# Kernel tuning notes

Hardware: AMD Instinct MI355X
Metric: run time of the kernel (lower is better)

## Reference

```python
import jax, jax.numpy as jnp
import numpy as np

S, G, NMUL, LENF = 730, 4000, 2, 15
NEARZERO = 1e-5

# param bounds (change_param_range: lb + raw*(ub-lb)), raw in [0,1]
HBV_LB = np.array([1., 50., .05, .01, .001, .2, 0., 0., -2.5, .5, 0., 0.], np.float32)
HBV_UB = np.array([6., 1000., .9, .5, .2, 1., 10., 100., 2.5, 10., .1, .2], np.float32)
EXP_LB = np.array([0., 100., 10., 0., 0., -3.], np.float32)
EXP_UB = np.array([.1, 1500., 50., 5., 3., 0.], np.float32)


def _descale(raw, lb, ub):
    # raw: [G, n_par, NMUL]
    return lb[None, :, None] + raw * (ub - lb)[None, :, None]


def _hbv(P, T, PET, ph):
    # ph: [G,12,NMUL]; order: beta fc k0 k1 k2 lp perc uzl tt cfmax cfr cwh
    beta, fc, k0, k1, k2, lp, perc, uzl, tt, cfmax, cfr, cwh = [ph[:, i, :] for i in range(12)]

    def step(carry, inp):
        sp, mw, sm, suz, slz = carry
        p, t, pet = inp
        rain = jnp.where(t >= tt, p, 0.)
        sp = sp + jnp.where(t < tt, p, 0.)
        melt = jnp.minimum(jnp.maximum(cfmax * (t - tt), 0.), sp)
        mw = mw + melt; sp = sp - melt
        refr = jnp.minimum(jnp.maximum(cfr * cfmax * (tt - t), 0.), mw)
        sp = sp + refr; mw = mw - refr
        tosoil = jnp.maximum(mw - cwh * sp, 0.)
        mw = mw - tosoil
        sw = jnp.clip((sm / fc) ** beta, 0., 1.)
        rech = (rain + tosoil) * sw
        sm = sm + rain + tosoil - rech
        excess = jnp.maximum(sm - fc, 0.); sm = sm - excess
        et = jnp.minimum(pet * jnp.clip(sm / (lp * fc), 0., 1.), sm)
        sm = jnp.maximum(sm - et, NEARZERO)
        suz = suz + rech + excess
        pa = jnp.minimum(perc, suz); suz = suz - pa
        q0 = k0 * jnp.maximum(suz - uzl, 0.); suz = suz - q0
        q1 = k1 * suz; suz = suz - q1
        slz = slz + pa
        q2 = k2 * slz; slz = slz - q2
        return (sp, mw, sm, suz, slz), q0 + q1 + q2

    z = jnp.full_like(fc, NEARZERO)
    init = (z, z, 0.5 * fc, z, z)
    _, q = jax.lax.scan(step, init, (P, T, PET))
    return q  # [S,G,NMUL]


def _exphydro(P, T, PET, pe):
    # pe: [G,6,NMUL]; order: f smax qmax df tmax tmin
    f, smax, qmax, df, tmax, tmin = [pe[:, i, :] for i in range(6)]

    def step(carry, inp):
        s0, s1 = carry
        p, t, pet = inp
        ps = jnp.where(t <= tmin, p, 0.)
        pr = p - ps
        melt = jnp.where(t > tmax, jnp.minimum(s0, df * (t - tmax)), 0.)
        s0 = s0 + ps - melt
        s1 = s1 + pr + melt
        qspill = jnp.maximum(s1 - smax, 0.); s1 = s1 - qspill
        et = jnp.minimum(pet * jnp.clip(s1 / smax, 0., 1.), s1); s1 = s1 - et
        qb = jnp.minimum(qmax * jnp.exp(-f * jnp.maximum(smax - s1, 0.)), s1)
        s1 = s1 - qb
        return (s0, s1), qspill + qb

    z = jnp.full_like(smax, NEARZERO)
    init = (z, 0.5 * smax)
    _, q = jax.lax.scan(step, init, (P, T, PET))
    return q  # [S,G,NMUL]


def _uh_gamma(a, b):
    # a,b: [G]; gamma-pdf unit hydrograph, lenF=LENF
    aa = jax.nn.relu(a) + 0.1
    th = jax.nn.relu(b) + 0.5
    t = jnp.arange(LENF, dtype=jnp.float32) + 0.5  # [LENF]
    logw = (-jax.scipy.special.gammaln(aa)[None, :] - aa[None, :] * jnp.log(th)[None, :]
            + (aa - 1.)[None, :] * jnp.log(t)[:, None] - t[:, None] / th[None, :])
    w = jnp.exp(logw)
    return w / w.sum(0, keepdims=True)  # [LENF,G]


def _route(q, w):
    # causal depthwise conv: out[t,g] = sum_k w[k,g] * q[t-k,g]
    qp = jnp.pad(q, ((LENF - 1, 0), (0, 0)))
    out = jnp.zeros_like(q)
    for k in range(LENF):
        out = out + w[k][None, :] * qp[LENF - 1 - k: LENF - 1 - k + q.shape[0]]
    return out


def setup_inputs() -> dict:
    key = jax.random.key(0)
    k1, k2 = jax.random.split(key)
    u = jax.random.uniform(k1, (S, G, 3), dtype=jnp.float32)
    # physical forcing ranges: prcp [0,10] mm/d, tmean [-10,20] C, pet [0,5] mm/d
    x = jnp.stack([u[..., 0] * 10., u[..., 1] * 30. - 10., u[..., 2] * 5.], axis=-1)
    raw_phy_static = jax.random.uniform(k2, (G, 18 * NMUL + 2), dtype=jnp.float32)
    return {"x": x, "raw_phy_static": raw_phy_static}


def reference(x, raw_phy_static):
    # unpack: [G, 18*NMUL] static block + 2 routing params
    static = raw_phy_static[:, :18 * NMUL].reshape(G, 18, NMUL)
    ph = _descale(static[:, :12, :], jnp.asarray(HBV_LB), jnp.asarray(HBV_UB))
    pe = _descale(static[:, 12:, :], jnp.asarray(EXP_LB), jnp.asarray(EXP_UB))
    route = raw_phy_static[:, 18 * NMUL:]
    rout_a = route[:, 0] * 2.9   # bounds [0, 2.9]
    rout_b = route[:, 1] * 6.5   # bounds [0, 6.5]

    P = jnp.broadcast_to(x[:, :, 0, None], (S, G, NMUL))
    T = jnp.broadcast_to(x[:, :, 1, None], (S, G, NMUL))
    PET = jnp.broadcast_to(x[:, :, 2, None], (S, G, NMUL))

    q_hbv = _hbv(P, T, PET, ph)
    q_exp = _exphydro(P, T, PET, pe)
    qsim = 0.5 * (q_hbv.mean(-1) + q_exp.mean(-1))  # blend over models, mean over nmul -> [S,G]

    w = _uh_gamma(rout_a, rout_b)
    return _route(qsim, w)  # [S,G] routed streamflow
```

## Files before the change

### kernel.cpp

```cpp
#include <hip/hip_runtime.h>

#define SS 730
#define GG 4000
#define LENF 15
#define PD 10
#define GPAD 4032
#define TT 10
#define QN ((size_t)SS * GG)

template<bool STORE4>
__global__ __launch_bounds__(64, 1) void hydro_scan(const float* __restrict__ x,
                                                    const float* __restrict__ raw,
                                                    float* __restrict__ qsim) {
    int tid = blockIdx.x * 64 + threadIdx.x;
    int g = tid % GPAD;
    int inst = tid / GPAD;
    if (g >= GG) return;
    int m = inst & 1;
    const float* xg = x + (size_t)g * 3;
    const float* pr = raw + (size_t)g * 38 + m;

    float* qp = qsim + (STORE4 ? (size_t)inst * QN : 0) + g;

    float pb[PD], tb[PD], eb[PD];
#pragma unroll
    for (int j = 0; j < PD; ++j) {
        const float* xn = xg + (size_t)j * (3 * GG);
        pb[j] = xn[0]; tb[j] = xn[1]; eb[j] = xn[2];
    }

    if (inst < 2) {
        float beta  = 1.0f   + pr[0]  * 5.0f;
        float fc    = 50.0f  + pr[2]  * 950.0f;
        float k0    = 0.05f  + pr[4]  * 0.85f;
        float k1    = 0.01f  + pr[6]  * 0.49f;
        float k2    = 0.001f + pr[8]  * 0.199f;
        float lp    = 0.2f   + pr[10] * 0.8f;
        float perc  =          pr[12] * 10.0f;
        float uzl   =          pr[14] * 100.0f;
        float tt    = -2.5f  + pr[16] * 5.0f;
        float cfmax = 0.5f   + pr[18] * 9.5f;
        float cfr   =          pr[20] * 0.1f;
        float cwh   =          pr[22] * 0.2f;
        float invfc   = 1.0f / fc;
        float invlpfc = 1.0f / (lp * fc);
        float cfrcf   = cfr * cfmax;

        float sp = 1e-5f, mw = 1e-5f, sm = 0.5f * fc, suz = 1e-5f, slz = 1e-5f;

        auto body = [&](float p, float tc, float pet) -> float {
            float sw = exp2f(beta * __log2f(sm * invfc));
            float rain = (tc >= tt) ? p : 0.0f;
            float snow = p - rain;
            sp += snow;
            float melt = fminf(fmaxf(cfmax * (tc - tt), 0.0f), sp);
            mw += melt; sp -= melt;
            float refr = fminf(fmaxf(cfrcf * (tt - tc), 0.0f), mw);
            sp += refr; mw -= refr;
            float tosoil = fmaxf(mw - cwh * sp, 0.0f);
            mw -= tosoil;
            float rt = rain + tosoil;
            float rech = rt * sw;
            sm += rt - rech;
            float excess = fmaxf(sm - fc, 0.0f);
            sm -= excess;
            float et = fminf(pet * fminf(sm * invlpfc, 1.0f), sm);
            sm = fmaxf(sm - et, 1e-5f);
            suz += rech + excess;
            float pa = fminf(perc, suz);
            suz -= pa;
            float q0 = k0 * fmaxf(suz - uzl, 0.0f);
            suz -= q0;
            float q1 = k1 * suz;
            suz -= q1;
            slz += pa;
            float q2 = k2 * slz;
            slz -= q2;
            return q0 + q1 + q2;
        };

        const float* xpre = xg + (size_t)PD * (3 * GG);
        for (int c = 0; c < SS / PD - 1; ++c) {
#pragma unroll
            for (int j = 0; j < PD; ++j) {
                float p = pb[j], tc = tb[j], pet = eb[j];
                pb[j] = xpre[0]; tb[j] = xpre[1]; eb[j] = xpre[2];
                xpre += 3 * GG;
                float q = body(p, tc, pet);
                if (STORE4) *qp = q; else atomicAdd(qp, 0.25f * q);
                qp += GG;
            }
        }
#pragma unroll
        for (int j = 0; j < PD; ++j) {
            float q = body(pb[j], tb[j], eb[j]);
            if (STORE4) *qp = q; else atomicAdd(qp, 0.25f * q);
            qp += GG;
        }
    } else {
        const float* pe = pr + 24;
        float f    =           pe[0]  * 0.1f;
        float smax = 100.0f  + pe[2]  * 1400.0f;
        float qmax = 10.0f   + pe[4]  * 40.0f;
        float df   =           pe[6]  * 5.0f;
        float tmax =           pe[8]  * 3.0f;
        float tmin = -3.0f   + pe[10] * 3.0f;
        float invsmax = 1.0f / smax;
        float fl = f * 1.44269504f;

        float s0 = 1e-5f, s1 = 0.5f * smax;

        auto body = [&](float p, float tc, float pet) -> float {
            float ps  = (tc <= tmin) ? p : 0.0f;
            float prr = p - ps;
            float mlt = (tc > tmax) ? fminf(s0, df * (tc - tmax)) : 0.0f;
            s0 += ps - mlt;
            s1 += prr + mlt;
            float qspill = fmaxf(s1 - smax, 0.0f);
            s1 -= qspill;
            float et = fminf(pet * (s1 * invsmax), s1);
            s1 -= et;
            float qb = fminf(qmax * exp2f(-fl * (smax - s1)), s1);
            s1 -= qb;
            return qspill + qb;
        };

        const float* xpre = xg + (size_t)PD * (3 * GG);
        for (int c = 0; c < SS / PD - 1; ++c) {
#pragma unroll
            for (int j = 0; j < PD; ++j) {
                float p = pb[j], tc = tb[j], pet = eb[j];
                pb[j] = xpre[0]; tb[j] = xpre[1]; eb[j] = xpre[2];
                xpre += 3 * GG;
                float q = body(p, tc, pet);
                if (STORE4) *qp = q; else atomicAdd(qp, 0.25f * q);
                qp += GG;
            }
        }
#pragma unroll
        for (int j = 0; j < PD; ++j) {
            float q = body(pb[j], tb[j], eb[j]);
            if (STORE4) *qp = q; else atomicAdd(qp, 0.25f * q);
            qp += GG;
        }
    }
}

__global__ __launch_bounds__(256) void uh_weights(const float* __restrict__ raw,
                                                  float* __restrict__ wbuf) {
    int g = blockIdx.x * 256 + threadIdx.x;
    if (g >= GG) return;
    float a = raw[(size_t)g * 38 + 36] * 2.9f;
    float b = raw[(size_t)g * 38 + 37] * 6.5f;
    float aa = fmaxf(a, 0.0f) + 0.1f;
    float th = fmaxf(b, 0.0f) + 0.5f;
    float am1 = aa - 1.0f;
    float invth = 1.0f / th;

    const float logt[LENF] = {
        -0.69314718f, 0.40546511f, 0.91629073f, 1.25276297f, 1.50407740f,
         1.70474809f, 1.87180218f, 2.01490302f, 2.14006616f, 2.25129180f,
         2.35137526f, 2.44234704f, 2.52572864f, 2.60268969f, 2.67414865f };

    float w[LENF];
    float s = 0.0f;
#pragma unroll
    for (int k = 0; k < LENF; ++k) {
        float tk = (float)k + 0.5f;
        w[k] = expf(am1 * logt[k] - tk * invth);
        s += w[k];
    }
    float scale = 0.25f / s;
#pragma unroll
    for (int k = 0; k < LENF; ++k)
        wbuf[(size_t)k * GG + g] = w[k] * scale;
}

template<int NB, bool WPRE>
__global__ __launch_bounds__(256) void hydro_route(const float* __restrict__ qsim,
                                                   const float* __restrict__ raw,
                                                   const float* __restrict__ wbuf,
                                                   float* __restrict__ out) {
    int idx = blockIdx.x * 256 + threadIdx.x;
    if (idx >= GG * (SS / TT)) return;
    int g = idx % GG;
    int c = idx / GG;
    int t0 = c * TT;

    float w[LENF];
    float scale;
    if (WPRE) {
#pragma unroll
        for (int k = 0; k < LENF; ++k)
            w[k] = wbuf[(size_t)k * GG + g];
        scale = 1.0f;
    } else {
        float a = raw[(size_t)g * 38 + 36] * 2.9f;
        float b = raw[(size_t)g * 38 + 37] * 6.5f;
        float aa = fmaxf(a, 0.0f) + 0.1f;
        float th = fmaxf(b, 0.0f) + 0.5f;
        float am1 = aa - 1.0f;
        float invth = 1.0f / th;
        const float logt[LENF] = {
            -0.69314718f, 0.40546511f, 0.91629073f, 1.25276297f, 1.50407740f,
             1.70474809f, 1.87180218f, 2.01490302f, 2.14006616f, 2.25129180f,
             2.35137526f, 2.44234704f, 2.52572864f, 2.60268969f, 2.67414865f };
        float s = 0.0f;
#pragma unroll
        for (int k = 0; k < LENF; ++k) {
            float tk = (float)k + 0.5f;
            w[k] = expf(am1 * logt[k] - tk * invth);
            s += w[k];
        }
        scale = (NB == 4 ? 0.25f : 1.0f) / s;
    }

    float v[TT + LENF - 1];
#pragma unroll
    for (int i = 0; i < TT + LENF - 1; ++i) {
        int tp = t0 - (LENF - 1) + i;
        float sv = 0.0f;
        if (tp >= 0) {
            const float* qb = qsim + (size_t)tp * GG + g;
            sv = qb[0];
            if (NB == 4) sv += qb[QN] + qb[2 * QN] + qb[3 * QN];
        }
        v[i] = sv;
    }
#pragma unroll
    for (int j = 0; j < TT; ++j) {
        float acc = 0.0f;
#pragma unroll
        for (int k = 0; k < LENF; ++k)
            acc += w[k] * v[j + (LENF - 1) - k];
        out[(size_t)(t0 + j) * GG + g] = (WPRE ? acc : acc * scale);
    }
}

extern "C" void kernel_launch(void* const* d_in, const int* in_sizes, int n_in,
                              void* d_out, int out_size, void* d_ws, size_t ws_size,
                              hipStream_t stream) {
    const float* x   = (const float*)d_in[0];
    const float* raw = (const float*)d_in[1];
    float* out  = (float*)d_out;
    float* qsim = (float*)d_ws;

    const size_t slices4 = 4 * QN * sizeof(float);
    const size_t wbytes  = (size_t)LENF * GG * sizeof(float);
    int rblocks = (GG * (SS / TT) + 255) / 256;

    if (ws_size >= slices4 + wbytes) {
        float* wbuf = qsim + 4 * QN;
        hydro_scan<true><<<(4 * GPAD) / 64, 64, 0, stream>>>(x, raw, qsim);
        uh_weights<<<(GG + 255) / 256, 256, 0, stream>>>(raw, wbuf);
        hydro_route<4, true><<<rblocks, 256, 0, stream>>>(qsim, raw, wbuf, out);
    } else if (ws_size >= slices4) {
        hydro_scan<true><<<(4 * GPAD) / 64, 64, 0, stream>>>(x, raw, qsim);
        hydro_route<4, false><<<rblocks, 256, 0, stream>>>(qsim, raw, nullptr, out);
    } else {
        hipMemsetAsync(qsim, 0, QN * sizeof(float), stream);
        hydro_scan<false><<<(4 * GPAD) / 64, 64, 0, stream>>>(x, raw, qsim);
        hydro_route<1, false><<<rblocks, 256, 0, stream>>>(qsim, raw, nullptr, out);
    }
}
```

Measured before the change: 115.2 us.

## Shorten recurrence dependency chains and use 32-bit offsets in hydro scan

Rewrites the HBV and EXP-HYDRO per-step bodies so that work depending only on the inputs (temperature deltas, melt and refreeze caps, ET factors) is computed off the state-carried chain. Clamps are folded into min/max forms, suz updates are merged with precomputed 1-k0 and k0*uzl, and the baseflow exponential takes a precomputed log offset. Pointer arithmetic is replaced by 32-bit integer offsets to cut 64-bit address math. The aim is a lower per-step latency on the serial scan. The cost is small floating-point rounding differences, and ET is now a multiplicative clamp whose equivalence relies on the state staying in range.

```diff
diff --git a/kernel.cpp b/kernel.cpp
--- a/kernel.cpp
+++ b/kernel.cpp
@@ -7,6 +7,7 @@
 #define GPAD 4032
 #define TT 10
 #define QN ((size_t)SS * GG)
+#define QNI ((int)(SS * GG))
 
 template<bool STORE4>
 __global__ __launch_bounds__(64, 1) void hydro_scan(const float* __restrict__ x,
@@ -17,16 +18,16 @@
     int inst = tid / GPAD;
     if (g >= GG) return;
     int m = inst & 1;
-    const float* xg = x + (size_t)g * 3;
     const float* pr = raw + (size_t)g * 38 + m;
 
-    float* qp = qsim + (STORE4 ? (size_t)inst * QN : 0) + g;
+    int xoff = g * 3;
+    int qoff = g + (STORE4 ? inst * QNI : 0);
 
     float pb[PD], tb[PD], eb[PD];
 #pragma unroll
     for (int j = 0; j < PD; ++j) {
-        const float* xn = xg + (size_t)j * (3 * GG);
-        pb[j] = xn[0]; tb[j] = xn[1]; eb[j] = xn[2];
+        pb[j] = x[xoff]; tb[j] = x[xoff + 1]; eb[j] = x[xoff + 2];
+        xoff += 3 * GG;
     }
 
     if (inst < 2) {
@@ -44,58 +45,67 @@
         float cwh   =          pr[22] * 0.2f;
         float invfc   = 1.0f / fc;
         float invlpfc = 1.0f / (lp * fc);
-        float cfrcf   = cfr * cfmax;
+        float ncfrcf  = -(cfr * cfmax);
+        float omk0    = 1.0f - k0;
+        float k0uzl   = k0 * uzl;
+        float omk1    = 1.0f - k1;
 
         float sp = 1e-5f, mw = 1e-5f, sm = 0.5f * fc, suz = 1e-5f, slz = 1e-5f;
 
         auto body = [&](float p, float tc, float pet) -> float {
-            float sw = exp2f(beta * __log2f(sm * invfc));
-            float rain = (tc >= tt) ? p : 0.0f;
+            float dt   = tc - tt;
+            float msn  = fmaxf(cfmax * dt, 0.0f);
+            float mrf  = fmaxf(ncfrcf * dt, 0.0f);
+            float rain = (dt >= 0.0f) ? p : 0.0f;
             float snow = p - rain;
-            sp += snow;
-            float melt = fminf(fmaxf(cfmax * (tc - tt), 0.0f), sp);
-            mw += melt; sp -= melt;
-            float refr = fminf(fmaxf(cfrcf * (tt - tc), 0.0f), mw);
-            sp += refr; mw -= refr;
-            float tosoil = fmaxf(mw - cwh * sp, 0.0f);
-            mw -= tosoil;
-            float rt = rain + tosoil;
-            float rech = rt * sw;
-            sm += rt - rech;
-            float excess = fmaxf(sm - fc, 0.0f);
-            sm -= excess;
-            float et = fminf(pet * fminf(sm * invlpfc, 1.0f), sm);
-            sm = fmaxf(sm - et, 1e-5f);
-            suz += rech + excess;
-            float pa = fminf(perc, suz);
-            suz -= pa;
-            float q0 = k0 * fmaxf(suz - uzl, 0.0f);
-            suz -= q0;
-            float q1 = k1 * suz;
-            suz -= q1;
-            slz += pa;
-            float q2 = k2 * slz;
-            slz -= q2;
-            return q0 + q1 + q2;
+            float etk  = fmaf(-invlpfc, pet, 1.0f);
+            float sw   = exp2f(beta * __log2f(sm * invfc));
+            float omsw = 1.0f - sw;
+            float sp1  = sp + snow;
+            float melt = fminf(msn, sp1);
+            float mw2  = mw + melt;
+            float sp2  = sp1 - melt;
+            float refr = fminf(mrf, mw2);
+            float mw3  = mw2 - refr;
+            sp = sp2 + refr;
+            float mw4  = fminf(mw3, cwh * sp);
+            float tosoil = mw3 - mw4;
+            mw = mw4;
+            float rt    = rain + tosoil;
+            float sm1   = fmaf(rt, omsw, sm);
+            float rech  = rt * sw;
+            float excess = fmaxf(sm1 - fc, 0.0f);
+            float sm2   = fminf(sm1, fc);
+            sm = fmaxf(fmaxf(sm2 * etk, sm2 - pet), 1e-5f);
+            float suz1 = suz + rech + excess;
+            float suz2 = fmaxf(suz1 - perc, 0.0f);
+            float pa   = suz1 - suz2;
+            float suz3 = fminf(suz2, fmaf(suz2, omk0, k0uzl));
+            float suzn = omk1 * suz3;
+            float q01  = suz2 - suzn;
+            suz = suzn;
+            float slz1 = slz + pa;
+            float q2   = k2 * slz1;
+            slz = slz1 - q2;
+            return q01 + q2;
         };
 
-        const float* xpre = xg + (size_t)PD * (3 * GG);
         for (int c = 0; c < SS / PD - 1; ++c) {
 #pragma unroll
             for (int j = 0; j < PD; ++j) {
                 float p = pb[j], tc = tb[j], pet = eb[j];
-                pb[j] = xpre[0]; tb[j] = xpre[1]; eb[j] = xpre[2];
-                xpre += 3 * GG;
+                pb[j] = x[xoff]; tb[j] = x[xoff + 1]; eb[j] = x[xoff + 2];
+                xoff += 3 * GG;
                 float q = body(p, tc, pet);
-                if (STORE4) *qp = q; else atomicAdd(qp, 0.25f * q);
-                qp += GG;
+                if (STORE4) qsim[qoff] = q; else atomicAdd(&qsim[qoff], 0.25f * q);
+                qoff += GG;
             }
         }
 #pragma unroll
         for (int j = 0; j < PD; ++j) {
             float q = body(pb[j], tb[j], eb[j]);
-            if (STORE4) *qp = q; else atomicAdd(qp, 0.25f * q);
-            qp += GG;
+            if (STORE4) qsim[qoff] = q; else atomicAdd(&qsim[qoff], 0.25f * q);
+            qoff += GG;
         }
     } else {
         const float* pe = pr + 24;
@@ -107,41 +117,42 @@
         float tmin = -3.0f   + pe[10] * 3.0f;
         float invsmax = 1.0f / smax;
         float fl = f * 1.44269504f;
+        float c0 = __log2f(qmax) - fl * smax;
 
         float s0 = 1e-5f, s1 = 0.5f * smax;
 
         auto body = [&](float p, float tc, float pet) -> float {
+            float mdf = df * fmaxf(tc - tmax, 0.0f);
             float ps  = (tc <= tmin) ? p : 0.0f;
             float prr = p - ps;
-            float mlt = (tc > tmax) ? fminf(s0, df * (tc - tmax)) : 0.0f;
-            s0 += ps - mlt;
-            s1 += prr + mlt;
-            float qspill = fmaxf(s1 - smax, 0.0f);
-            s1 -= qspill;
-            float et = fminf(pet * (s1 * invsmax), s1);
-            s1 -= et;
-            float qb = fminf(qmax * exp2f(-fl * (smax - s1)), s1);
-            s1 -= qb;
+            float etk = fmaxf(fmaf(-invsmax, pet, 1.0f), 0.0f);
+            float mlt = fminf(s0, mdf);
+            s0 = fmaxf(s0 - mdf, 0.0f) + ps;
+            float s1a = s1 + prr + mlt;
+            float qspill = fmaxf(s1a - smax, 0.0f);
+            float s1b = fminf(s1a, smax);
+            float s1c = s1b * etk;
+            float qb  = fminf(exp2f(fmaf(fl, s1c, c0)), s1c);
+            s1 = s1c - qb;
             return qspill + qb;
         };
 
-        const float* xpre = xg + (size_t)PD * (3 * GG);
         for (int c = 0; c < SS / PD - 1; ++c) {
 #pragma unroll
             for (int j = 0; j < PD; ++j) {
                 float p = pb[j], tc = tb[j], pet = eb[j];
-                pb[j] = xpre[0]; tb[j] = xpre[1]; eb[j] = xpre[2];
-                xpre += 3 * GG;
+                pb[j] = x[xoff]; tb[j] = x[xoff + 1]; eb[j] = x[xoff + 2];
+                xoff += 3 * GG;
                 float q = body(p, tc, pet);
-                if (STORE4) *qp = q; else atomicAdd(qp, 0.25f * q);
-                qp += GG;
+                if (STORE4) qsim[qoff] = q; else atomicAdd(&qsim[qoff], 0.25f * q);
+                qoff += GG;
             }
         }
 #pragma unroll
         for (int j = 0; j < PD; ++j) {
             float q = body(pb[j], tb[j], eb[j]);
-            if (STORE4) *qp = q; else atomicAdd(qp, 0.25f * q);
-            qp += GG;
+            if (STORE4) qsim[qoff] = q; else atomicAdd(&qsim[qoff], 0.25f * q);
+            qoff += GG;
         }
     }
 }
```

Result: faster. 111.2 us (-3.5%).
